# Kernel tuning notes

Hardware: AMD Instinct MI355X
Metric: run time of the kernel (lower is better)

Reference implementation:

```python
import jax, jax.numpy as jnp
import numpy as np

D_MODEL = 1024
N_HEADS = 16
K_RETRIEVED = 32
BANK_SIZE = 131072
EPS = 1e-12  # matches F.normalize eps


def setup_inputs() -> dict:
    key = jax.random.key(0)
    ks = jax.random.split(key, 7)
    B, T = 8, 2048
    x = jax.random.normal(ks[0], (B, T, D_MODEL), dtype=jnp.float32)
    mem_keys = jax.random.normal(ks[1], (BANK_SIZE, D_MODEL), dtype=jnp.float32)
    mem_values = jax.random.normal(ks[2], (BANK_SIZE, D_MODEL), dtype=jnp.float32)
    s = 1.0 / np.sqrt(D_MODEL)
    Wq = jax.random.normal(ks[3], (D_MODEL, D_MODEL), dtype=jnp.float32) * s
    Wk = jax.random.normal(ks[4], (D_MODEL, D_MODEL), dtype=jnp.float32) * s
    Wv = jax.random.normal(ks[5], (D_MODEL, D_MODEL), dtype=jnp.float32) * s
    Wo = jax.random.normal(ks[6], (D_MODEL, D_MODEL), dtype=jnp.float32) * s
    gate_logit = jnp.zeros((1,), dtype=jnp.float32)
    return {"x": x, "mem_keys": mem_keys, "mem_values": mem_values,
            "Wq": Wq, "Wk": Wk, "Wv": Wv, "Wo": Wo, "gate_logit": gate_logit}


def _normalize(v):
    n = jnp.linalg.norm(v, axis=-1, keepdims=True)
    return v / jnp.maximum(n, EPS)


def reference(x, mem_keys, mem_values, Wq, Wk, Wv, Wo, gate_logit):
    B, T, D = x.shape
    H, hd, k = N_HEADS, D_MODEL // N_HEADS, K_RETRIEVED

    # --- retrieval: mean-pool query, cosine-sim top-k, gather values ---
    q = x.mean(axis=1)                       # (B, D)
    sims = _normalize(q) @ _normalize(mem_keys).T   # (B, BANK_SIZE)
    _, idx = jax.lax.top_k(sims, k)          # (B, k) descending
    retrieved = mem_values[idx]              # (B, k, d_mem)

    # --- cross-attention over retrieved docs ---
    Q = (x @ Wq).reshape(B, T, H, hd)
    K = (retrieved @ Wk).reshape(B, k, H, hd)
    V = (retrieved @ Wv).reshape(B, k, H, hd)
    scale = 1.0 / jnp.sqrt(jnp.asarray(hd, dtype=x.dtype))
    attn = jnp.einsum('bthd,bkhd->bhtk', Q, K) * scale
    attn = jax.nn.softmax(attn, axis=-1)
    ctx = jnp.einsum('bhtk,bkhd->bthd', attn, V).reshape(B, T, D)
    ctx = ctx @ Wo

    gate = jax.nn.sigmoid(gate_logit)        # (1,) broadcasts
    return x + gate * ctx
```

## Files before the change

kernel.cpp:

```cpp
#include <hip/hip_runtime.h>

#define D_MODEL 1024
#define NH 16
#define HD 64
#define KRET 32
#define BANK 131072
#define BB 8
#define TT 2048
#define MTOK 16384
#define EPSN 1e-12f

typedef __attribute__((ext_vector_type(8))) short bf16x8;
typedef __attribute__((ext_vector_type(8))) unsigned short u16x8;
typedef __attribute__((ext_vector_type(4))) float f32x4;

__device__ __forceinline__ unsigned short f2bf(float f) {
  unsigned int u = __float_as_uint(f);
  u += 0x7fffu + ((u >> 16) & 1u);
  return (unsigned short)(u >> 16);
}
__device__ __forceinline__ float bf2f(unsigned short h) {
  return __uint_as_float(((unsigned int)h) << 16);
}

__device__ __forceinline__ void gload16(const void* g, void* l) {
  __builtin_amdgcn_global_load_lds(
      (const __attribute__((address_space(1))) unsigned int*)g,
      (__attribute__((address_space(3))) unsigned int*)l, 16, 0, 0);
}

__global__ __launch_bounds__(256) void k_prep(const float* __restrict__ x,
                                              unsigned short* __restrict__ xb,
                                              float* __restrict__ part,
                                              const float* W0, const float* W1,
                                              const float* W2, const float* W3,
                                              unsigned short* T0, unsigned short* T1,
                                              unsigned short* T2, unsigned short* T3) {
  __shared__ float tile[64][65];
  int id = blockIdx.x, tid = threadIdx.x;
  if (id < 512) {
    int ch = id & 63, b = id >> 6;
    const float4* xp = (const float4*)(x + ((size_t)b * TT + ch * 32) * D_MODEL);
    ushort4* xo = (ushort4*)(xb + ((size_t)b * TT + ch * 32) * D_MODEL);
    float4 acc = {0.f, 0.f, 0.f, 0.f};
#pragma unroll 4
    for (int t = 0; t < 32; t++) {
      float4 v = xp[t * 256 + tid];
      acc.x += v.x; acc.y += v.y; acc.z += v.z; acc.w += v.w;
      ushort4 o;
      o.x = f2bf(v.x); o.y = f2bf(v.y); o.z = f2bf(v.z); o.w = f2bf(v.w);
      xo[t * 256 + tid] = o;
    }
    ((float4*)part)[((size_t)b * 64 + ch) * 256 + tid] = acc;
  } else {
    int wid = id - 512;
    int nx = wid & 15, ny = (wid >> 4) & 15, nz = wid >> 8;
    const float* W; unsigned short* T;
    switch (nz) {
      case 0: W = W0; T = T0; break;
      case 1: W = W1; T = T1; break;
      case 2: W = W2; T = T2; break;
      default: W = W3; T = T3; break;
    }
    int k0 = ny * 64, n0 = nx * 64;
#pragma unroll
    for (int i = 0; i < 16; i++) {
      int idx = tid + i * 256; int r = idx >> 6, c = idx & 63;
      tile[r][c] = W[(size_t)(k0 + r) * D_MODEL + n0 + c];
    }
    __syncthreads();
#pragma unroll
    for (int i = 0; i < 16; i++) {
      int idx = tid + i * 256; int r = idx >> 6, c = idx & 63;
      T[(size_t)(n0 + r) * D_MODEL + k0 + c] = f2bf(tile[c][r]);
    }
  }
}

__global__ __launch_bounds__(256) void k_qnorm(const float* __restrict__ part,
                                               float* __restrict__ qn) {
  int b = blockIdx.x; int tid = threadIdx.x;
  __shared__ float red[4];
  const float4* pp = (const float4*)part + (size_t)b * 64 * 256 + tid;
  float4 a = {0.f, 0.f, 0.f, 0.f};
#pragma unroll 8
  for (int p = 0; p < 64; p++) {
    float4 v = pp[(size_t)p * 256];
    a.x += v.x; a.y += v.y; a.z += v.z; a.w += v.w;
  }
  const float sc = 1.f / (float)TT;
  a.x *= sc; a.y *= sc; a.z *= sc; a.w *= sc;
  float ss = a.x * a.x + a.y * a.y + a.z * a.z + a.w * a.w;
#pragma unroll
  for (int m = 32; m >= 1; m >>= 1) ss += __shfl_xor(ss, m);
  if ((tid & 63) == 0) red[tid >> 6] = ss;
  __syncthreads();
  float tot = red[0] + red[1] + red[2] + red[3];
  float inv = 1.f / fmaxf(sqrtf(tot), EPSN);
  float4 o = {a.x * inv, a.y * inv, a.z * inv, a.w * inv};
  ((float4*)qn)[(size_t)b * 256 + tid] = o;
}

__global__ __launch_bounds__(256) void k_sims(const float* __restrict__ mk,
                                              const float* __restrict__ qn,
                                              float* __restrict__ sims) {
  int wave = threadIdx.x >> 6, lane = threadIdx.x & 63;
  int row0 = (blockIdx.x * 4 + wave) * 4;
  float4 kv[4][4];
#pragma unroll
  for (int r = 0; r < 4; r++) {
    const float4* kr = (const float4*)(mk + (size_t)(row0 + r) * D_MODEL);
#pragma unroll
    for (int i = 0; i < 4; i++) kv[r][i] = kr[lane + 64 * i];
  }
  float ss[4] = {0.f, 0.f, 0.f, 0.f};
#pragma unroll
  for (int r = 0; r < 4; r++)
#pragma unroll
    for (int i = 0; i < 4; i++)
      ss[r] += kv[r][i].x * kv[r][i].x + kv[r][i].y * kv[r][i].y +
               kv[r][i].z * kv[r][i].z + kv[r][i].w * kv[r][i].w;
  float dots[8][4];
#pragma unroll
  for (int b = 0; b < 8; b++)
#pragma unroll
    for (int r = 0; r < 4; r++) dots[b][r] = 0.f;
#pragma unroll
  for (int b = 0; b < 8; b++) {
    const float4* qb = (const float4*)(qn + (size_t)b * D_MODEL);
#pragma unroll
    for (int i = 0; i < 4; i++) {
      float4 q4 = qb[lane + 64 * i];
#pragma unroll
      for (int r = 0; r < 4; r++)
        dots[b][r] += kv[r][i].x * q4.x + kv[r][i].y * q4.y +
                      kv[r][i].z * q4.z + kv[r][i].w * q4.w;
    }
  }
#pragma unroll
  for (int m = 32; m >= 1; m >>= 1) {
#pragma unroll
    for (int r = 0; r < 4; r++) ss[r] += __shfl_xor(ss[r], m);
#pragma unroll
    for (int b = 0; b < 8; b++)
#pragma unroll
      for (int r = 0; r < 4; r++) dots[b][r] += __shfl_xor(dots[b][r], m);
  }
  if (lane == 0) {
#pragma unroll
    for (int r = 0; r < 4; r++) {
      float inv = 1.f / fmaxf(sqrtf(ss[r]), EPSN);
#pragma unroll
      for (int b = 0; b < 8; b++)
        sims[(size_t)b * BANK + row0 + r] = dots[b][r] * inv;
    }
  }
}

__global__ __launch_bounds__(256) void k_topk_local(const float* __restrict__ sims,
                                                    float* __restrict__ cval,
                                                    int* __restrict__ cidx) {
  int b = blockIdx.y, chunk = blockIdx.x;
  int tid = threadIdx.x, wave = tid >> 6, lane = tid & 63;
  const float* sb = sims + (size_t)b * BANK + chunk * 2048;
  float v[8]; int gi[8];
#pragma unroll
  for (int j = 0; j < 8; j++) {
    int loc = j * 256 + tid;
    v[j] = sb[loc];
    gi[j] = chunk * 2048 + loc;
  }
  __shared__ float wv[4]; __shared__ int wi[4];
  __shared__ int bcast;
  for (int it = 0; it < KRET; ++it) {
    float best = -1e30f; int besti = 1 << 30;
#pragma unroll
    for (int j = 0; j < 8; j++)
      if (v[j] > best || (v[j] == best && gi[j] < besti)) { best = v[j]; besti = gi[j]; }
#pragma unroll
    for (int m = 32; m >= 1; m >>= 1) {
      float ov = __shfl_xor(best, m); int oi = __shfl_xor(besti, m);
      if (ov > best || (ov == best && oi < besti)) { best = ov; besti = oi; }
    }
    if (lane == 0) { wv[wave] = best; wi[wave] = besti; }
    __syncthreads();
    if (tid == 0) {
      float fb = wv[0]; int fi = wi[0];
      for (int w = 1; w < 4; w++)
        if (wv[w] > fb || (wv[w] == fb && wi[w] < fi)) { fb = wv[w]; fi = wi[w]; }
      bcast = fi;
      cval[((size_t)b * 64 + chunk) * KRET + it] = fb;
      cidx[((size_t)b * 64 + chunk) * KRET + it] = fi;
    }
    __syncthreads();
    int w = bcast;
#pragma unroll
    for (int j = 0; j < 8; j++)
      if (gi[j] == w) v[j] = -1e30f;
  }
}

__global__ __launch_bounds__(256) void k_topk_merge(const float* __restrict__ cval,
                                                    const int* __restrict__ cidx,
                                                    int* __restrict__ idx) {
  int b = blockIdx.x;
  int tid = threadIdx.x, wave = tid >> 6, lane = tid & 63;
  const float* cv = cval + (size_t)b * 2048;
  const int* ci = cidx + (size_t)b * 2048;
  float v[8]; int gi[8];
#pragma unroll
  for (int j = 0; j < 8; j++) {
    int loc = j * 256 + tid;
    v[j] = cv[loc];
    gi[j] = ci[loc];
  }
  __shared__ float wv[4]; __shared__ int wi[4];
  __shared__ int bcast;
  for (int it = 0; it < KRET; ++it) {
    float best = -1e30f; int besti = 1 << 30;
#pragma unroll
    for (int j = 0; j < 8; j++)
      if (v[j] > best || (v[j] == best && gi[j] < besti)) { best = v[j]; besti = gi[j]; }
#pragma unroll
    for (int m = 32; m >= 1; m >>= 1) {
      float ov = __shfl_xor(best, m); int oi = __shfl_xor(besti, m);
      if (ov > best || (ov == best && oi < besti)) { best = ov; besti = oi; }
    }
    if (lane == 0) { wv[wave] = best; wi[wave] = besti; }
    __syncthreads();
    if (tid == 0) {
      float fb = wv[0]; int fi = wi[0];
      for (int w = 1; w < 4; w++)
        if (wv[w] > fb || (wv[w] == fb && wi[w] < fi)) { fb = wv[w]; fi = wi[w]; }
      bcast = fi;
      idx[b * KRET + it] = fi;
    }
    __syncthreads();
    int w = bcast;
#pragma unroll
    for (int j = 0; j < 8; j++)
      if (gi[j] == w) v[j] = -1e30f;
  }
}

__global__ __launch_bounds__(256) void k_kvgemm(const float* __restrict__ mv,
                                                const int* __restrict__ idx_g,
                                                const unsigned short* __restrict__ Bt,
                                                float* __restrict__ Kout,
                                                float* __restrict__ Vout) {
  __shared__ __align__(16) unsigned short As[128 * 32];
  __shared__ __align__(16) unsigned short Bs[128 * 32];
  __shared__ int idxs[128];
  const int tid = threadIdx.x;
  const int wave = tid >> 6, lane = tid & 63;
  const int bm = blockIdx.x * 128, bn = blockIdx.y * 128;
  const int wm = (wave >> 1) * 64, wn = (wave & 1) * 64;
  const int frow = lane & 15, kg = lane >> 4;
  const int K = 1024;

  if (tid < 128) idxs[tid] = idx_g[bm + tid];
  __syncthreads();

  f32x4 acc[4][4] = {};

  const int row0 = tid >> 2, col0 = (tid & 3) * 8;
  const int row1 = row0 + 64;
  const int g0 = tid * 8;
  const int g1 = 2048 + tid * 8;
  const unsigned short* b0 = Bt + (size_t)(bn + (g0 >> 5)) * K + (g0 & 31);
  const unsigned short* b1 = Bt + (size_t)(bn + (g1 >> 5)) * K + (g1 & 31);
  unsigned short* lB0 = &Bs[wave * 512];
  unsigned short* lB1 = &Bs[2048 + wave * 512];
  const float* src0 = mv + (size_t)idxs[row0] * D_MODEL + col0;
  const float* src1 = mv + (size_t)idxs[row1] * D_MODEL + col0;

  for (int k0 = 0; k0 < K; k0 += 32) {
    gload16(b0 + k0, lB0);
    gload16(b1 + k0, lB1);
    float4 u0 = *(const float4*)(src0 + k0);
    float4 w0 = *(const float4*)(src0 + k0 + 4);
    float4 u1 = *(const float4*)(src1 + k0);
    float4 w1 = *(const float4*)(src1 + k0 + 4);
    u16x8 p0, p1;
    p0[0] = f2bf(u0.x); p0[1] = f2bf(u0.y); p0[2] = f2bf(u0.z); p0[3] = f2bf(u0.w);
    p0[4] = f2bf(w0.x); p0[5] = f2bf(w0.y); p0[6] = f2bf(w0.z); p0[7] = f2bf(w0.w);
    p1[0] = f2bf(u1.x); p1[1] = f2bf(u1.y); p1[2] = f2bf(u1.z); p1[3] = f2bf(u1.w);
    p1[4] = f2bf(w1.x); p1[5] = f2bf(w1.y); p1[6] = f2bf(w1.z); p1[7] = f2bf(w1.w);
    *(u16x8*)&As[row0 * 32 + col0] = p0;
    *(u16x8*)&As[row1 * 32 + col0] = p1;
    __syncthreads();
    bf16x8 fa[4], fb[4];
#pragma unroll
    for (int i = 0; i < 4; i++)
      fa[i] = *(const bf16x8*)&As[(wm + i * 16 + frow) * 32 + kg * 8];
#pragma unroll
    for (int i = 0; i < 4; i++)
      fb[i] = *(const bf16x8*)&Bs[(wn + i * 16 + frow) * 32 + kg * 8];
#pragma unroll
    for (int i = 0; i < 4; i++)
#pragma unroll
      for (int j = 0; j < 4; j++)
        acc[i][j] = __builtin_amdgcn_mfma_f32_16x16x32_bf16(fa[i], fb[j], acc[i][j], 0, 0, 0);
    __syncthreads();
  }

  const int crow = (lane >> 4) * 4, ccol = lane & 15;
#pragma unroll
  for (int i = 0; i < 4; i++)
#pragma unroll
    for (int j = 0; j < 4; j++)
#pragma unroll
      for (int r = 0; r < 4; r++) {
        int gm = bm + wm + i * 16 + crow + r;
        int gn = bn + wn + j * 16 + ccol;
        int b = gm >> 5, jj = gm & 31;
        if (gn < 1024) {
          int h = gn >> 6, d = gn & 63;
          Kout[((((size_t)b * NH + h) * KRET + jj) << 6) + d] = acc[i][j][r];
        } else {
          int gn2 = gn - 1024;
          int h = gn2 >> 6, d = gn2 & 63;
          Vout[((((size_t)b * NH + h) * KRET + jj) << 6) + d] = acc[i][j][r];
        }
      }
}

#define LDSA(SB) (LDS + (SB) * 8192)
#define LDSB(SB) (LDS + 32768 + (SB) * 8192)
#define STG_A(SB, T)                                  \
  do {                                                \
    const int st_ = (T) < 31 ? (T) : 31;              \
    gload16(aS0 + st_ * 32, LDSA(SB) + ldst0);        \
    gload16(aS1 + st_ * 32, LDSA(SB) + ldst1);        \
  } while (0)
#define STG_B(SB, T)                                  \
  do {                                                \
    const int st_ = (T) < 31 ? (T) : 31;              \
    gload16(bS0 + st_ * 32, LDSB(SB) + ldst0);        \
    gload16(bS1 + st_ * 32, LDSB(SB) + ldst1);        \
  } while (0)
#define GPH(CB, I0, NEWB, STMT, VM)                                            \
  do {                                                                         \
    bf16x8 af[4];                                                              \
    _Pragma("unroll") for (int ii = 0; ii < 4; ii++)                           \
        af[ii] = *(const bf16x8*)(LDSA(CB) + ((wr * 128 + (I0 + ii) * 16 + fr) << 5) + (sA << 3)); \
    if (NEWB) {                                                                \
      _Pragma("unroll") for (int jj = 0; jj < 4; jj++)                         \
          bf[jj] = *(const bf16x8*)(LDSB(CB) + ((wc * 64 + jj * 16 + fr) << 5) + (sA << 3)); \
    }                                                                          \
    STMT;                                                                      \
    __builtin_amdgcn_s_barrier();                                              \
    __builtin_amdgcn_s_setprio(1);                                             \
    _Pragma("unroll") for (int ii = 0; ii < 4; ii++)                           \
        _Pragma("unroll") for (int jj = 0; jj < 4; jj++)                       \
            acc[I0 + ii][jj] = __builtin_amdgcn_mfma_f32_16x16x32_bf16(        \
                af[ii], bf[jj], acc[I0 + ii][jj], 0, 0, 0);                    \
    __builtin_amdgcn_s_setprio(0);                                             \
    if (VM) asm volatile("s_waitcnt vmcnt(4)" ::: "memory");                   \
    __builtin_amdgcn_s_barrier();                                              \
  } while (0)
#define GEMM_KLOOP(Ap, Bp)                                                      \
  const int r0 = tid >> 2, s0 = tid & 3;                                        \
  const int sw0 = s0 ^ ((r0 >> 1) & 3);                                         \
  const int r1 = r0 + 128;                                                      \
  const int sw1 = s0 ^ ((r1 >> 1) & 3);                                         \
  const unsigned short* aS0 = (Ap) + (size_t)(bm + r0) * 1024 + sw0 * 8;        \
  const unsigned short* aS1 = (Ap) + (size_t)(bm + r1) * 1024 + sw1 * 8;        \
  const unsigned short* bS0 = (Bp) + (size_t)(bn + r0) * 1024 + sw0 * 8;        \
  const unsigned short* bS1 = (Bp) + (size_t)(bn + r1) * 1024 + sw1 * 8;        \
  const int ldst0 = wid << 9;                                                   \
  const int ldst1 = 4096 + (wid << 9);                                          \
  const int sA = kg ^ ((fr >> 1) & 3);                                          \
  STG_A(0, 0); STG_B(0, 0);                                                     \
  STG_A(1, 1); STG_B(1, 1);                                                     \
  STG_A(2, 2); STG_B(2, 2);                                                     \
  asm volatile("s_waitcnt vmcnt(4)" ::: "memory");                              \
  __builtin_amdgcn_s_barrier();                                                 \
  _Pragma("unroll 1") for (int it = 0; it < 8; ++it) {                          \
    const int t = it * 4;                                                       \
    GPH(0, 0, 1, STG_A(3, t + 3), 0);                                           \
    GPH(0, 4, 0, STG_B(3, t + 3), 0);                                           \
    GPH(1, 0, 1, STG_A(0, t + 4), 0);                                           \
    GPH(1, 4, 0, STG_B(0, t + 4), 1);                                           \
    GPH(2, 0, 1, STG_A(1, t + 5), 0);                                           \
    GPH(2, 4, 0, STG_B(1, t + 5), 0);                                           \
    GPH(3, 0, 1, STG_A(2, t + 6), 0);                                           \
    GPH(3, 4, 0, STG_B(2, t + 6), 1);                                           \
  }

__global__ __launch_bounds__(512, 2) void k_qattn(const unsigned short* __restrict__ A,
                                                  const unsigned short* __restrict__ Bt,
                                                  const float* __restrict__ Kws,
                                                  const float* __restrict__ Vws,
                                                  unsigned short* __restrict__ ctx) {
  __shared__ __align__(16) unsigned short LDS[65536];
  const int tid = threadIdx.x;
  const int wid = tid >> 6, lane = tid & 63;
  const int wr = wid >> 2, wc = wid & 3;
  const int fr = lane & 15, kg = lane >> 4;
  const int bm = blockIdx.x * 256, bn = blockIdx.y * 256;

  f32x4 acc[8][4] = {};
  bf16x8 bf[4];

  GEMM_KLOOP(A, Bt)

  asm volatile("s_waitcnt vmcnt(0)" ::: "memory");
  __syncthreads();

  unsigned short* Kl = LDS;
  unsigned short* Vt = LDS + 9216;
  unsigned short* Qs = LDS + 19456;
  unsigned short* Pl = LDS + 28672;
  const int b = bm >> 11;
  const int hbase = blockIdx.y * 4;
  {
    int hq = tid >> 7, rem = tid & 127, doc = rem >> 2, dq = (rem & 3) * 16;
    const float4* kp = (const float4*)(Kws + ((((size_t)b * NH + hbase + hq) * KRET + doc) << 6) + dq);
    float4 k0 = kp[0], k1 = kp[1], k2 = kp[2], k3 = kp[3];
    u16x8 ka, kb2;
    ka[0] = f2bf(k0.x); ka[1] = f2bf(k0.y); ka[2] = f2bf(k0.z); ka[3] = f2bf(k0.w);
    ka[4] = f2bf(k1.x); ka[5] = f2bf(k1.y); ka[6] = f2bf(k1.z); ka[7] = f2bf(k1.w);
    kb2[0] = f2bf(k2.x); kb2[1] = f2bf(k2.y); kb2[2] = f2bf(k2.z); kb2[3] = f2bf(k2.w);
    kb2[4] = f2bf(k3.x); kb2[5] = f2bf(k3.y); kb2[6] = f2bf(k3.z); kb2[7] = f2bf(k3.w);
    *(u16x8*)&Kl[hq * 2304 + doc * 72 + dq] = ka;
    *(u16x8*)&Kl[hq * 2304 + doc * 72 + dq + 8] = kb2;
    const float4* vp = (const float4*)(Vws + ((((size_t)b * NH + hbase + hq) * KRET + doc) << 6) + dq);
    float4 v0 = vp[0], v1 = vp[1], v2 = vp[2], v3 = vp[3];
    float vv[16] = {v0.x, v0.y, v0.z, v0.w, v1.x, v1.y, v1.z, v1.w,
                    v2.x, v2.y, v2.z, v2.w, v3.x, v3.y, v3.z, v3.w};
#pragma unroll
    for (int j = 0; j < 16; j++) Vt[hq * 2560 + (dq + j) * 40 + doc] = f2bf(vv[j]);
  }
  __syncthreads();

  unsigned short* Klh = Kl + wc * 2304;
  unsigned short* Vth = Vt + wc * 2560;
  const bf16x8 kb00 = *(const bf16x8*)&Klh[fr * 72 + kg * 8];
  const bf16x8 kb01 = *(const bf16x8*)&Klh[fr * 72 + 32 + kg * 8];
  const bf16x8 kb10 = *(const bf16x8*)&Klh[(16 + fr) * 72 + kg * 8];
  const bf16x8 kb11 = *(const bf16x8*)&Klh[(16 + fr) * 72 + 32 + kg * 8];
  bf16x8 vbf[4];
#pragma unroll
  for (int dt = 0; dt < 4; dt++)
    vbf[dt] = *(const bf16x8*)&Vth[(dt * 16 + fr) * 40 + kg * 8];
  unsigned short* Qw = Qs + wid * 1152;
  unsigned short* pw = Pl + wid * 640;
  const int h = hbase + wc;

#pragma unroll
  for (int i = 0; i < 8; ++i) {
#pragma unroll
    for (int j = 0; j < 4; j++)
#pragma unroll
      for (int r = 0; r < 4; r++)
        Qw[(kg * 4 + r) * 72 + j * 16 + fr] = f2bf(acc[i][j][r]);
    asm volatile("s_waitcnt lgkmcnt(0)" ::: "memory");
    bf16x8 qa0 = *(const bf16x8*)&Qw[fr * 72 + kg * 8];
    bf16x8 qa1 = *(const bf16x8*)&Qw[fr * 72 + 32 + kg * 8];
    f32x4 s0 = {}, s1 = {};
    s0 = __builtin_amdgcn_mfma_f32_16x16x32_bf16(qa0, kb00, s0, 0, 0, 0);
    s0 = __builtin_amdgcn_mfma_f32_16x16x32_bf16(qa1, kb01, s0, 0, 0, 0);
    s1 = __builtin_amdgcn_mfma_f32_16x16x32_bf16(qa0, kb10, s1, 0, 0, 0);
    s1 = __builtin_amdgcn_mfma_f32_16x16x32_bf16(qa1, kb11, s1, 0, 0, 0);
    float a0[4], a1[4], mr[4], e0[4], e1[4], sr[4];
#pragma unroll
    for (int r = 0; r < 4; r++) {
      a0[r] = s0[r] * 0.125f; a1[r] = s1[r] * 0.125f;
      mr[r] = fmaxf(a0[r], a1[r]);
    }
#pragma unroll
    for (int m = 1; m < 16; m <<= 1)
#pragma unroll
      for (int r = 0; r < 4; r++) mr[r] = fmaxf(mr[r], __shfl_xor(mr[r], m));
#pragma unroll
    for (int r = 0; r < 4; r++) {
      e0[r] = __expf(a0[r] - mr[r]); e1[r] = __expf(a1[r] - mr[r]);
      sr[r] = e0[r] + e1[r];
    }
#pragma unroll
    for (int m = 1; m < 16; m <<= 1)
#pragma unroll
      for (int r = 0; r < 4; r++) sr[r] += __shfl_xor(sr[r], m);
#pragma unroll
    for (int r = 0; r < 4; r++) {
      float inv = 1.f / sr[r];
      int tl = kg * 4 + r;
      pw[tl * 40 + fr] = f2bf(e0[r] * inv);
      pw[tl * 40 + 16 + fr] = f2bf(e1[r] * inv);
    }
    asm volatile("s_waitcnt lgkmcnt(0)" ::: "memory");
    bf16x8 pa = *(const bf16x8*)&pw[fr * 40 + kg * 8];
    f32x4 c[4];
#pragma unroll
    for (int dt = 0; dt < 4; dt++) {
      f32x4 z = {};
      c[dt] = __builtin_amdgcn_mfma_f32_16x16x32_bf16(pa, vbf[dt], z, 0, 0, 0);
    }
#pragma unroll
    for (int r = 0; r < 4; r++) {
      int tl = kg * 4 + r;
      unsigned short* crow = ctx + ((size_t)(bm + wr * 128 + i * 16 + tl)) * D_MODEL + h * HD;
#pragma unroll
      for (int dt = 0; dt < 4; dt++)
        crow[dt * 16 + fr] = f2bf(c[dt][r]);
    }
  }
}

__global__ __launch_bounds__(512, 2) void k_gemmO(const unsigned short* __restrict__ A,
                                                  const unsigned short* __restrict__ Bt,
                                                  float* __restrict__ out_f,
                                                  const float* __restrict__ xres,
                                                  const float* __restrict__ gatep) {
  __shared__ __align__(16) unsigned short LDS[65536];
  const int tid = threadIdx.x;
  const int wid = tid >> 6, lane = tid & 63;
  const int wr = wid >> 2, wc = wid & 3;
  const int fr = lane & 15, kg = lane >> 4;
  const int bm = blockIdx.x * 256, bn = blockIdx.y * 256;

  f32x4 acc[8][4] = {};
  bf16x8 bf[4];

  GEMM_KLOOP(A, Bt)

  const int crow = kg * 4, ccol = fr;
  float gate = 1.f / (1.f + __expf(-gatep[0]));
#pragma unroll
  for (int i = 0; i < 8; i++)
#pragma unroll
    for (int j = 0; j < 4; j++)
#pragma unroll
      for (int r = 0; r < 4; r++) {
        int gm = bm + wr * 128 + i * 16 + crow + r;
        int gn = bn + wc * 64 + j * 16 + ccol;
        size_t off = (size_t)gm * D_MODEL + gn;
        out_f[off] = xres[off] + gate * acc[i][j][r];
      }
}

extern "C" void kernel_launch(void* const* d_in, const int* in_sizes, int n_in,
                              void* d_out, int out_size, void* d_ws, size_t ws_size,
                              hipStream_t stream) {
  const float* x = (const float*)d_in[0];
  const float* mk = (const float*)d_in[1];
  const float* mv = (const float*)d_in[2];
  const float* Wq = (const float*)d_in[3];
  const float* Wk = (const float*)d_in[4];
  const float* Wv = (const float*)d_in[5];
  const float* Wo = (const float*)d_in[6];
  const float* gatep = (const float*)d_in[7];
  float* out = (float*)d_out;

  char* ws = (char*)d_ws;
  unsigned short* xb   = (unsigned short*)(ws);
  unsigned short* ctxb = (unsigned short*)(ws + 33554432);
  unsigned short* WqT  = (unsigned short*)(ws + 67108864);
  unsigned short* WkvT = (unsigned short*)(ws + 69206016);
  unsigned short* WoT  = (unsigned short*)(ws + 73400320);
  float* qn    = (float*)(ws + 75497472);
  float* sims  = (float*)(ws + 75530240);
  float* part  = (float*)(ws + 75530240);
  int*   idx   = (int*)(ws + 79724544);
  float* cval  = (float*)(ws + 79725568);
  int*   cidxb = (int*)(ws + 79791104);
  float* Kws   = (float*)(ws + 79856640);
  float* Vws   = (float*)(ws + 80905216);

  k_prep<<<dim3(1536), 256, 0, stream>>>(x, xb, part, Wq, Wk, Wv, Wo,
                                         WqT, WkvT, WkvT + 1048576, WoT);
  k_qnorm<<<dim3(8), 256, 0, stream>>>(part, qn);
  k_sims<<<dim3(BANK / 16), 256, 0, stream>>>(mk, qn, sims);
  k_topk_local<<<dim3(64, 8), 256, 0, stream>>>(sims, cval, cidxb);
  k_topk_merge<<<dim3(8), 256, 0, stream>>>(cval, cidxb, idx);
  k_kvgemm<<<dim3(2, 16), 256, 0, stream>>>(mv, idx, WkvT, Kws, Vws);
  k_qattn<<<dim3(64, 4), 512, 0, stream>>>(xb, WqT, Kws, Vws, ctxb);
  k_gemmO<<<dim3(64, 4), 512, 0, stream>>>(ctxb, WoT, out, x, gatep);
}
```

Baseline: 405.1 us.

## Fuse retrieved K/V projection into the Q-attention kernel epilogue

```diff
diff --git a/kernel.cpp b/kernel.cpp
--- a/kernel.cpp
+++ b/kernel.cpp
@@ -241,88 +241,6 @@
     for (int j = 0; j < 8; j++)
       if (gi[j] == w) v[j] = -1e30f;
   }
-}
-
-__global__ __launch_bounds__(256) void k_kvgemm(const float* __restrict__ mv,
-                                                const int* __restrict__ idx_g,
-                                                const unsigned short* __restrict__ Bt,
-                                                float* __restrict__ Kout,
-                                                float* __restrict__ Vout) {
-  __shared__ __align__(16) unsigned short As[128 * 32];
-  __shared__ __align__(16) unsigned short Bs[128 * 32];
-  __shared__ int idxs[128];
-  const int tid = threadIdx.x;
-  const int wave = tid >> 6, lane = tid & 63;
-  const int bm = blockIdx.x * 128, bn = blockIdx.y * 128;
-  const int wm = (wave >> 1) * 64, wn = (wave & 1) * 64;
-  const int frow = lane & 15, kg = lane >> 4;
-  const int K = 1024;
-
-  if (tid < 128) idxs[tid] = idx_g[bm + tid];
-  __syncthreads();
-
-  f32x4 acc[4][4] = {};
-
-  const int row0 = tid >> 2, col0 = (tid & 3) * 8;
-  const int row1 = row0 + 64;
-  const int g0 = tid * 8;
-  const int g1 = 2048 + tid * 8;
-  const unsigned short* b0 = Bt + (size_t)(bn + (g0 >> 5)) * K + (g0 & 31);
-  const unsigned short* b1 = Bt + (size_t)(bn + (g1 >> 5)) * K + (g1 & 31);
-  unsigned short* lB0 = &Bs[wave * 512];
-  unsigned short* lB1 = &Bs[2048 + wave * 512];
-  const float* src0 = mv + (size_t)idxs[row0] * D_MODEL + col0;
-  const float* src1 = mv + (size_t)idxs[row1] * D_MODEL + col0;
-
-  for (int k0 = 0; k0 < K; k0 += 32) {
-    gload16(b0 + k0, lB0);
-    gload16(b1 + k0, lB1);
-    float4 u0 = *(const float4*)(src0 + k0);
-    float4 w0 = *(const float4*)(src0 + k0 + 4);
-    float4 u1 = *(const float4*)(src1 + k0);
-    float4 w1 = *(const float4*)(src1 + k0 + 4);
-    u16x8 p0, p1;
-    p0[0] = f2bf(u0.x); p0[1] = f2bf(u0.y); p0[2] = f2bf(u0.z); p0[3] = f2bf(u0.w);
-    p0[4] = f2bf(w0.x); p0[5] = f2bf(w0.y); p0[6] = f2bf(w0.z); p0[7] = f2bf(w0.w);
-    p1[0] = f2bf(u1.x); p1[1] = f2bf(u1.y); p1[2] = f2bf(u1.z); p1[3] = f2bf(u1.w);
-    p1[4] = f2bf(w1.x); p1[5] = f2bf(w1.y); p1[6] = f2bf(w1.z); p1[7] = f2bf(w1.w);
-    *(u16x8*)&As[row0 * 32 + col0] = p0;
-    *(u16x8*)&As[row1 * 32 + col0] = p1;
-    __syncthreads();
-    bf16x8 fa[4], fb[4];
-#pragma unroll
-    for (int i = 0; i < 4; i++)
-      fa[i] = *(const bf16x8*)&As[(wm + i * 16 + frow) * 32 + kg * 8];
-#pragma unroll
-    for (int i = 0; i < 4; i++)
-      fb[i] = *(const bf16x8*)&Bs[(wn + i * 16 + frow) * 32 + kg * 8];
-#pragma unroll
-    for (int i = 0; i < 4; i++)
-#pragma unroll
-      for (int j = 0; j < 4; j++)
-        acc[i][j] = __builtin_amdgcn_mfma_f32_16x16x32_bf16(fa[i], fb[j], acc[i][j], 0, 0, 0);
-    __syncthreads();
-  }
-
-  const int crow = (lane >> 4) * 4, ccol = lane & 15;
-#pragma unroll
-  for (int i = 0; i < 4; i++)
-#pragma unroll
-    for (int j = 0; j < 4; j++)
-#pragma unroll
-      for (int r = 0; r < 4; r++) {
-        int gm = bm + wm + i * 16 + crow + r;
-        int gn = bn + wn + j * 16 + ccol;
-        int b = gm >> 5, jj = gm & 31;
-        if (gn < 1024) {
-          int h = gn >> 6, d = gn & 63;
-          Kout[((((size_t)b * NH + h) * KRET + jj) << 6) + d] = acc[i][j][r];
-        } else {
-          int gn2 = gn - 1024;
-          int h = gn2 >> 6, d = gn2 & 63;
-          Vout[((((size_t)b * NH + h) * KRET + jj) << 6) + d] = acc[i][j][r];
-        }
-      }
 }
 
 #define LDSA(SB) (LDS + (SB) * 8192)
@@ -390,10 +308,12 @@
 
 __global__ __launch_bounds__(512, 2) void k_qattn(const unsigned short* __restrict__ A,
                                                   const unsigned short* __restrict__ Bt,
-                                                  const float* __restrict__ Kws,
-                                                  const float* __restrict__ Vws,
+                                                  const float* __restrict__ mv,
+                                                  const int* __restrict__ idx_g,
+                                                  const unsigned short* __restrict__ WkvT,
                                                   unsigned short* __restrict__ ctx) {
   __shared__ __align__(16) unsigned short LDS[65536];
+  __shared__ int idxs_sh[KRET];
   const int tid = threadIdx.x;
   const int wid = tid >> 6, lane = tid & 63;
   const int wr = wid >> 2, wc = wid & 3;
@@ -414,23 +334,52 @@
   unsigned short* Pl = LDS + 28672;
   const int b = bm >> 11;
   const int hbase = blockIdx.y * 4;
+
+  if (tid < KRET) idxs_sh[tid] = idx_g[b * KRET + tid];
+  __syncthreads();
   {
-    int hq = tid >> 7, rem = tid & 127, doc = rem >> 2, dq = (rem & 3) * 16;
-    const float4* kp = (const float4*)(Kws + ((((size_t)b * NH + hbase + hq) * KRET + doc) << 6) + dq);
-    float4 k0 = kp[0], k1 = kp[1], k2 = kp[2], k3 = kp[3];
-    u16x8 ka, kb2;
-    ka[0] = f2bf(k0.x); ka[1] = f2bf(k0.y); ka[2] = f2bf(k0.z); ka[3] = f2bf(k0.w);
-    ka[4] = f2bf(k1.x); ka[5] = f2bf(k1.y); ka[6] = f2bf(k1.z); ka[7] = f2bf(k1.w);
-    kb2[0] = f2bf(k2.x); kb2[1] = f2bf(k2.y); kb2[2] = f2bf(k2.z); kb2[3] = f2bf(k2.w);
-    kb2[4] = f2bf(k3.x); kb2[5] = f2bf(k3.y); kb2[6] = f2bf(k3.z); kb2[7] = f2bf(k3.w);
-    *(u16x8*)&Kl[hq * 2304 + doc * 72 + dq] = ka;
-    *(u16x8*)&Kl[hq * 2304 + doc * 72 + dq + 8] = kb2;
-    const float4* vp = (const float4*)(Vws + ((((size_t)b * NH + hbase + hq) * KRET + doc) << 6) + dq);
-    float4 v0 = vp[0], v1 = vp[1], v2 = vp[2], v3 = vp[3];
-    float vv[16] = {v0.x, v0.y, v0.z, v0.w, v1.x, v1.y, v1.z, v1.w,
-                    v2.x, v2.y, v2.z, v2.w, v3.x, v3.y, v3.z, v3.w};
-#pragma unroll
-    for (int j = 0; j < 16; j++) Vt[hq * 2560 + (dq + j) * 40 + doc] = f2bf(vv[j]);
+    const int isV = wid >> 2;
+    const int nbase = (wid & 3) * 64;
+    const unsigned short* Bkv = WkvT + ((size_t)isV * 1048576) +
+                                ((size_t)(hbase * HD + nbase)) * 1024;
+#pragma unroll
+    for (int dt = 0; dt < 2; ++dt) {
+      const float* arow = mv + (size_t)idxs_sh[dt * 16 + fr] * D_MODEL;
+      f32x4 ak[4] = {};
+#pragma unroll 4
+      for (int k0 = 0; k0 < 1024; k0 += 32) {
+        float4 fa0 = *(const float4*)(arow + k0 + kg * 8);
+        float4 fa1 = *(const float4*)(arow + k0 + kg * 8 + 4);
+        u16x8 afr;
+        afr[0] = f2bf(fa0.x); afr[1] = f2bf(fa0.y); afr[2] = f2bf(fa0.z); afr[3] = f2bf(fa0.w);
+        afr[4] = f2bf(fa1.x); afr[5] = f2bf(fa1.y); afr[6] = f2bf(fa1.z); afr[7] = f2bf(fa1.w);
+        bf16x8 afb = *(bf16x8*)&afr;
+#pragma unroll
+        for (int ct = 0; ct < 4; ct++) {
+          bf16x8 bb = *(const bf16x8*)&Bkv[(size_t)(ct * 16 + fr) * 1024 + k0 + kg * 8];
+          ak[ct] = __builtin_amdgcn_mfma_f32_16x16x32_bf16(afb, bb, ak[ct], 0, 0, 0);
+        }
+      }
+      if (!isV) {
+#pragma unroll
+        for (int ct = 0; ct < 4; ct++)
+#pragma unroll
+          for (int r = 0; r < 4; r++) {
+            int doc = dt * 16 + kg * 4 + r;
+            int ncol = nbase + ct * 16 + fr;
+            Kl[(ncol >> 6) * 2304 + doc * 72 + (ncol & 63)] = f2bf(ak[ct][r]);
+          }
+      } else {
+#pragma unroll
+        for (int ct = 0; ct < 4; ct++)
+#pragma unroll
+          for (int r = 0; r < 4; r++) {
+            int doc = dt * 16 + kg * 4 + r;
+            int ncol = nbase + ct * 16 + fr;
+            Vt[(ncol >> 6) * 2560 + (ncol & 63) * 40 + doc] = f2bf(ak[ct][r]);
+          }
+      }
+    }
   }
   __syncthreads();
 
@@ -565,8 +514,6 @@
   int*   idx   = (int*)(ws + 79724544);
   float* cval  = (float*)(ws + 79725568);
   int*   cidxb = (int*)(ws + 79791104);
-  float* Kws   = (float*)(ws + 79856640);
-  float* Vws   = (float*)(ws + 80905216);
 
   k_prep<<<dim3(1536), 256, 0, stream>>>(x, xb, part, Wq, Wk, Wv, Wo,
                                          WqT, WkvT, WkvT + 1048576, WoT);
@@ -574,7 +521,6 @@
   k_sims<<<dim3(BANK / 16), 256, 0, stream>>>(mk, qn, sims);
   k_topk_local<<<dim3(64, 8), 256, 0, stream>>>(sims, cval, cidxb);
   k_topk_merge<<<dim3(8), 256, 0, stream>>>(cval, cidxb, idx);
-  k_kvgemm<<<dim3(2, 16), 256, 0, stream>>>(mv, idx, WkvT, Kws, Vws);
-  k_qattn<<<dim3(64, 4), 512, 0, stream>>>(xb, WqT, Kws, Vws, ctxb);
+  k_qattn<<<dim3(64, 4), 512, 0, stream>>>(xb, WqT, mv, idx, WkvT, ctxb);
   k_gemmO<<<dim3(64, 4), 512, 0, stream>>>(ctxb, WoT, out, x, gatep);
 }
```

Result: slower. 476.1 us (+17.5%).
